# Kernel optimization log

Hardware: AMD Instinct MI355X
Metric: run time of the kernel (lower is better)

Reference implementation:

```python
import jax, jax.numpy as jnp
import numpy as np

# Model constants (from init_kwargs)
N_ATOMS = 30000
N_PAIRS = 300000
NF_IN = 64
NF_OUT = 64
N_DIST = 20
MIND_SOFT = 0.85
MAXD_SOFT = 5.0
HARD_CUTOFF = 6.5


def setup_inputs() -> dict:
    key = jax.random.key(0)
    k = jax.random.split(key, 8)
    in_features = jax.random.normal(k[0], (N_ATOMS, NF_IN), dtype=jnp.float32)
    pair_first = jax.random.randint(k[1], (N_PAIRS,), 0, N_ATOMS)
    pair_second = jax.random.randint(k[2], (N_PAIRS,), 0, N_ATOMS)
    dist_pairs = jax.random.uniform(k[3], (N_PAIRS,), dtype=jnp.float32,
                                    minval=MIND_SOFT, maxval=HARD_CUTOFF)
    # InverseSensitivityModule init: mu uniformly spaced in inverse-distance space
    mu = jnp.linspace(1.0 / MAXD_SOFT, 1.0 / MIND_SOFT, N_DIST, dtype=jnp.float32)
    sigma = jnp.full((N_DIST,), (1.0 / MIND_SOFT - 1.0 / MAXD_SOFT) / N_DIST,
                     dtype=jnp.float32)
    # xavier-normal-ish init scales
    int_weights = jax.random.normal(k[4], (N_DIST, NF_OUT, NF_IN), dtype=jnp.float32) \
        * np.sqrt(2.0 / (NF_IN + NF_OUT)).astype(np.float32)
    w_self = jax.random.normal(k[5], (NF_OUT, NF_IN), dtype=jnp.float32) \
        * np.sqrt(2.0 / (NF_IN + NF_OUT)).astype(np.float32)
    b_self = jax.random.normal(k[6], (NF_OUT,), dtype=jnp.float32) * 0.01
    return {"in_features": in_features, "pair_first": pair_first,
            "pair_second": pair_second, "dist_pairs": dist_pairs,
            "mu": mu, "sigma": sigma, "int_weights": int_weights,
            "w_self": w_self, "b_self": b_self}


def _sensitivity(dist, mu, sigma):
    # Inverse-distance Gaussian sensitivities with smooth cosine hard cutoff.
    inv_d = 1.0 / dist  # [P]
    gauss = jnp.exp(-0.5 * ((inv_d[:, None] - mu[None, :]) / sigma[None, :]) ** 2)  # [P, n_dist]
    cut = jnp.cos(0.5 * jnp.pi * dist / HARD_CUTOFF) ** 2
    cut = jnp.where(dist < HARD_CUTOFF, cut, 0.0)
    return gauss * cut[:, None]


def reference(in_features, pair_first, pair_second, dist_pairs,
              mu, sigma, int_weights, w_self, b_self):
    n_atoms = in_features.shape[0]
    sense = _sensitivity(dist_pairs, mu, sigma)              # [P, n_dist]
    # envsum: env[a, nu, f] = sum_{p: pair_first[p]==a} sense[p, nu] * in_features[pair_second[p], f]
    neigh = in_features[pair_second]                          # [P, nf_in] gather
    contrib = sense[:, :, None] * neigh[:, None, :]           # [P, n_dist, nf_in]
    env = jax.ops.segment_sum(
        contrib.reshape(contrib.shape[0], N_DIST * NF_IN),
        pair_first, num_segments=n_atoms)                     # [A, n_dist*nf_in]
    # interaction matmul: weights permuted (n_dist, nf_in, nf_out) then flattened
    weights_rs = jnp.transpose(int_weights, (0, 2, 1)).reshape(N_DIST * NF_IN, NF_OUT)
    features_out = env @ weights_rs                           # [A, nf_out]
    features_out += in_features @ w_self.T + b_self           # self interaction
    return features_out
```

## Files before the change

### kernel.cpp

```cpp
#include <hip/hip_runtime.h>
#include <math.h>

#define N_ATOMS    30000
#define N_PAIRS    300000
#define CAP        48
#define NF         64
#define ND         20
#define K_ENV      1280
#define K_TOT      1344
#define NKSTEP     42
#define BA         8
#define ESTRIDE    1352
#define D_LO       0.85f
#define D_SCALE    (5.65f / 65535.0f)
#define D_SCALE_I  (65535.0f / 5.65f)
#define NM1        ((unsigned)(N_ATOMS - 1))
#define PAD_WORD   0x0000FFFFu
#define GCONST     0.8493218f

typedef short    s16x8  __attribute__((ext_vector_type(8)));
typedef __bf16   bf16x8 __attribute__((ext_vector_type(8)));
typedef unsigned u32x4  __attribute__((ext_vector_type(4)));
typedef float    f32x4  __attribute__((ext_vector_type(4)));
typedef float    f32x16 __attribute__((ext_vector_type(16)));

__device__ __forceinline__ unsigned short f2bf(float x) {
    union { float f; unsigned u; } v; v.f = x;
    unsigned r = v.u + 0x7fffu + ((v.u >> 16) & 1u);
    return (unsigned short)(r >> 16);
}
__device__ __forceinline__ unsigned pkbf(float a, float b) {
    return (unsigned)f2bf(a) | ((unsigned)f2bf(b) << 16);
}
__device__ __forceinline__ unsigned pkrh(float a, float b) {
    unsigned ua = __builtin_bit_cast(unsigned, a) + 0x8000u;
    unsigned ub = __builtin_bit_cast(unsigned, b) + 0x8000u;
    return __builtin_amdgcn_perm(ub, ua, 0x07060302u);
}
__device__ __forceinline__ float senseq(unsigned pu, float slog, float nms) {
    float uf  = (float)(pu & 0xffffu);
    float d   = __builtin_fmaf(uf, D_SCALE, D_LO);
    float inv = __builtin_amdgcn_rcpf(d);
    float rev = __builtin_fmaf(uf, (float)(D_SCALE / 13.0f), D_LO / 13.0f);
    float cut = __builtin_fmaf(__builtin_amdgcn_cosf(rev), 0.5f, 0.5f);
    float zs  = __builtin_fmaf(inv, slog, nms);
    return __builtin_amdgcn_exp2f(-(zs * zs)) * cut;
}

__global__ void k_prep(const float* __restrict__ iw, const float* __restrict__ wself,
                       const float* __restrict__ mu, const float* __restrict__ sigma,
                       const float* __restrict__ x,
                       unsigned short* __restrict__ WtB, int* __restrict__ cnts,
                       float2* __restrict__ msr, unsigned* __restrict__ xb16,
                       unsigned* __restrict__ pk) {
    if (blockIdx.x < 42) {
        int idx = blockIdx.x * 256 + threadIdx.x;
        if (idx >= NKSTEP * 4 * 64) return;
        int l  = idx & 63;
        int q  = (idx >> 6) & 3;
        int ks = idx >> 8;
        int n  = q * 16 + (l & 15);
        int kb = ks * 32 + (l >> 4) * 8;
        u32x4 u;
        #pragma unroll
        for (int jj = 0; jj < 4; jj++) {
            unsigned short lo, hi;
            #pragma unroll
            for (int e = 0; e < 2; e++) {
                int k = kb + 2 * jj + e;
                float val;
                if (k < K_ENV) {
                    int t  = k / 640;
                    int rm = k - t * 640;
                    int g  = rm >> 7;
                    int c  = (rm & 127) >> 2;
                    int r  = k & 3;
                    int nu = 4 * g + r;
                    int f  = 2 * c + t;
                    val = iw[(nu * NF + n) * NF + f];
                } else {
                    val = wself[n * NF + (k - K_ENV)];
                }
                if (e == 0) lo = f2bf(val); else hi = f2bf(val);
            }
            u[jj] = (unsigned)lo | ((unsigned)hi << 16);
        }
        *(u32x4*)&WtB[idx * 8] = u;
    } else if (blockIdx.x < 160) {
        int i = (blockIdx.x - 42) * 256 + threadIdx.x;
        if (i < N_ATOMS) cnts[i] = 0;
    } else if (blockIdx.x == 160) {
        int i = threadIdx.x;
        if (i < ND) {
            float isg = 1.0f / sigma[i];
            float2 m;
            m.y = isg * GCONST;
            m.x = -mu[i] * isg * GCONST;
            msr[i] = m;
        }
    } else if (blockIdx.x < 1099) {
        int o = (blockIdx.x - 161) * 256 + threadIdx.x;
        if (o < N_ATOMS * 32 / 4) {
            int wbase = o * 4;
            const float* src = &x[(size_t)wbase * 2];
            float2 f0 = *(const float2*)(src);
            float2 f1 = *(const float2*)(src + 2);
            float2 f2 = *(const float2*)(src + 4);
            float2 f3 = *(const float2*)(src + 6);
            u32x4 u;
            u[0] = pkbf(f0.x, f0.y);
            u[1] = pkbf(f1.x, f1.y);
            u[2] = pkbf(f2.x, f2.y);
            u[3] = pkbf(f3.x, f3.y);
            *(u32x4*)&xb16[wbase] = u;
        }
    } else {
        int o = (blockIdx.x - 1099) * 256 + threadIdx.x;
        if (o < N_ATOMS * CAP / 4) {
            u32x4 u = {PAD_WORD, PAD_WORD, PAD_WORD, PAD_WORD};
            *(u32x4*)&pk[(size_t)o * 4] = u;
        }
    }
}

__global__ void k_scatter(const int* __restrict__ first, const int* __restrict__ second,
                          const float* __restrict__ dist, int* __restrict__ cnts,
                          unsigned* __restrict__ pk) {
    int p = (blockIdx.x * 256 + threadIdx.x) * 2;
    if (p >= N_PAIRS) return;
    int2   f2 = *(const int2*)&first[p];
    int2   s2 = *(const int2*)&second[p];
    float2 d2 = *(const float2*)&dist[p];
    {
        int pos = atomicAdd(&cnts[f2.x], 1);
        if (pos < CAP) {
            unsigned du = min((unsigned)((d2.x - D_LO) * D_SCALE_I + 0.5f), 65535u);
            pk[(size_t)f2.x * CAP + pos] = ((unsigned)s2.x << 16) | du;
        }
    }
    {
        int pos = atomicAdd(&cnts[f2.y], 1);
        if (pos < CAP) {
            unsigned du = min((unsigned)((d2.y - D_LO) * D_SCALE_I + 0.5f), 65535u);
            pk[(size_t)f2.y * CAP + pos] = ((unsigned)s2.y << 16) | du;
        }
    }
}

__global__ void __launch_bounds__(512, 6)
k_main(const unsigned* __restrict__ xb16, const int* __restrict__ cnts,
       const unsigned* __restrict__ pk, const float2* __restrict__ msr,
       const unsigned short* __restrict__ WtB, const float* __restrict__ bself,
       float* __restrict__ out) {
    __shared__ unsigned short env[BA * ESTRIDE];
    const int t  = threadIdx.x;
    const int w  = t >> 6;
    const int l  = t & 63;
    const int h  = l >> 5;
    const int cl = l & 31;
    const int a  = blockIdx.x * BA + w;

    float2 ms = msr[min(cl, ND - 1)];
    const float slog = ms.y;
    const float nms  = ms.x;
    const unsigned* xw = xb16 + cl;

    const int cnt = min(cnts[a], CAP);
    const int nst = (cnt + 15) >> 4;
    const unsigned* gb = &pk[(size_t)a * CAP];
    f32x16 acc0 = {0.f}, acc1 = {0.f};
    #pragma unroll 1
    for (int ks = 0; ks < nst; ks++) {
        const int k0 = ks * 16 + h * 8;
        uint4 p0 = *(const uint4*)(gb + k0);
        uint4 p1 = *(const uint4*)(gb + k0 + 4);
        unsigned g0 = xw[min(p0.x >> 16, NM1) * 32];
        unsigned g1 = xw[min(p0.y >> 16, NM1) * 32];
        unsigned g2 = xw[min(p0.z >> 16, NM1) * 32];
        unsigned g3 = xw[min(p0.w >> 16, NM1) * 32];
        unsigned g4 = xw[min(p1.x >> 16, NM1) * 32];
        unsigned g5 = xw[min(p1.y >> 16, NM1) * 32];
        unsigned g6 = xw[min(p1.z >> 16, NM1) * 32];
        unsigned g7 = xw[min(p1.w >> 16, NM1) * 32];
        u32x4 A, B0, B1;
        A[0] = pkrh(senseq(p0.x, slog, nms), senseq(p0.y, slog, nms));
        A[1] = pkrh(senseq(p0.z, slog, nms), senseq(p0.w, slog, nms));
        A[2] = pkrh(senseq(p1.x, slog, nms), senseq(p1.y, slog, nms));
        A[3] = pkrh(senseq(p1.z, slog, nms), senseq(p1.w, slog, nms));
        B0[0] = __builtin_amdgcn_perm(g1, g0, 0x05040100u);
        B0[1] = __builtin_amdgcn_perm(g3, g2, 0x05040100u);
        B0[2] = __builtin_amdgcn_perm(g5, g4, 0x05040100u);
        B0[3] = __builtin_amdgcn_perm(g7, g6, 0x05040100u);
        B1[0] = __builtin_amdgcn_perm(g1, g0, 0x07060302u);
        B1[1] = __builtin_amdgcn_perm(g3, g2, 0x07060302u);
        B1[2] = __builtin_amdgcn_perm(g5, g4, 0x07060302u);
        B1[3] = __builtin_amdgcn_perm(g7, g6, 0x07060302u);
        acc0 = __builtin_amdgcn_mfma_f32_32x32x16_bf16(
                   __builtin_bit_cast(bf16x8, A),
                   __builtin_bit_cast(bf16x8, B0), acc0, 0, 0, 0);
        acc1 = __builtin_amdgcn_mfma_f32_32x32x16_bf16(
                   __builtin_bit_cast(bf16x8, A),
                   __builtin_bit_cast(bf16x8, B1), acc1, 0, 0, 0);
    }
    unsigned short* er = &env[w * ESTRIDE];
    #pragma unroll
    for (int q = 0; q < 3; q++) {
        int g = 2 * q + h;
        if (g < 5) {
            uint2 v0, v1;
            v0.x = pkrh(acc0[4 * q + 0], acc0[4 * q + 1]);
            v0.y = pkrh(acc0[4 * q + 2], acc0[4 * q + 3]);
            v1.x = pkrh(acc1[4 * q + 0], acc1[4 * q + 1]);
            v1.y = pkrh(acc1[4 * q + 2], acc1[4 * q + 3]);
            *(uint2*)&er[g * 128 + cl * 4]       = v0;
            *(uint2*)&er[640 + g * 128 + cl * 4] = v1;
        }
    }
    unsigned sw = xb16[(size_t)a * 32 + (l >> 1)];
    er[K_ENV + l] = (unsigned short)(sw >> ((l & 1) * 16));
    __syncthreads();

    if (w < 4) {
        const int m16  = l & 15;
        const int quad = l >> 4;
        f32x4 acc = {0.f, 0.f, 0.f, 0.f};
        for (int ks = 0; ks < NKSTEP; ks++) {
            s16x8 afrag = *(const s16x8*)&env[(m16 & 7) * ESTRIDE + ks * 32 + quad * 8];
            s16x8 bfrag = *(const s16x8*)&WtB[((ks * 4 + w) * 64 + l) * 8];
            acc = __builtin_amdgcn_mfma_f32_16x16x32_bf16(
                      __builtin_bit_cast(bf16x8, afrag),
                      __builtin_bit_cast(bf16x8, bfrag), acc, 0, 0, 0);
        }
        const float bs = bself[w * 16 + m16];
        const int a0 = blockIdx.x * BA;
        #pragma unroll
        for (int r = 0; r < 4; r++) {
            int row = quad * 4 + r;
            if (row < BA)
                out[(size_t)(a0 + row) * NF + w * 16 + m16] = acc[r] + bs;
        }
    }
}

extern "C" void kernel_launch(void* const* d_in, const int* in_sizes, int n_in,
                              void* d_out, int out_size, void* d_ws, size_t ws_size,
                              hipStream_t stream) {
    const float* x      = (const float*)d_in[0];
    const int*   first  = (const int*)d_in[1];
    const int*   second = (const int*)d_in[2];
    const float* dist   = (const float*)d_in[3];
    const float* mu     = (const float*)d_in[4];
    const float* sigma  = (const float*)d_in[5];
    const float* iw     = (const float*)d_in[6];
    const float* wself  = (const float*)d_in[7];
    const float* bself  = (const float*)d_in[8];
    float* out = (float*)d_out;

    char* ws = (char*)d_ws;
    unsigned short* WtB  = (unsigned short*)(ws);
    int*            cnts = (int*)(ws + 172032);
    float2*         msr  = (float2*)(ws + 292032);
    unsigned*       pk   = (unsigned*)(ws + 292192);
    unsigned*       xb16 = (unsigned*)(ws + 6052192);

    k_prep<<<dim3(1099 + (N_ATOMS * CAP / 4 + 255) / 256), dim3(256), 0, stream>>>(
        iw, wself, mu, sigma, x, WtB, cnts, msr, xb16, pk);
    k_scatter<<<dim3((N_PAIRS / 2 + 255) / 256), dim3(256), 0, stream>>>(
        first, second, dist, cnts, pk);
    k_main<<<dim3(N_ATOMS / BA), dim3(512), 0, stream>>>(
        xb16, cnts, pk, msr, WtB, bself, out);
}
```

Before: 130.9 us.

## Use persistent blocks with atomic tile queue, 16-atom tiles, and masked padding

The main kernel now runs a fixed grid of persistent blocks that pull 16-atom tiles from an atomic counter. Each wave builds environments for two atoms, so the second-stage 16x16 MFMA uses all 16 rows instead of 8. The per-call pass that wrote 0xFFFF padding words into the neighbour list is removed; sensitivities for slots past each atom's count are zeroed in registers instead. This saves a large memset and wasted MFMA rows, at the cost of an extra atomic and barrier per tile and larger shared memory per block.

Result: slower. 190.7 us (+45.7%).

```diff
diff --git a/kernel.cpp b/kernel.cpp
--- a/kernel.cpp
+++ b/kernel.cpp
@@ -9,13 +9,14 @@
 #define K_ENV      1280
 #define K_TOT      1344
 #define NKSTEP     42
-#define BA         8
+#define BA         16
+#define NTILE      1875
+#define NBLK       768
 #define ESTRIDE    1352
 #define D_LO       0.85f
 #define D_SCALE    (5.65f / 65535.0f)
 #define D_SCALE_I  (65535.0f / 5.65f)
 #define NM1        ((unsigned)(N_ATOMS - 1))
-#define PAD_WORD   0x0000FFFFu
 #define GCONST     0.8493218f
 
 typedef short    s16x8  __attribute__((ext_vector_type(8)));
@@ -37,14 +38,16 @@
     unsigned ub = __builtin_bit_cast(unsigned, b) + 0x8000u;
     return __builtin_amdgcn_perm(ub, ua, 0x07060302u);
 }
-__device__ __forceinline__ float senseq(unsigned pu, float slog, float nms) {
+__device__ __forceinline__ float senseq(unsigned pu, int kidx, int cnt,
+                                        float slog, float nms) {
     float uf  = (float)(pu & 0xffffu);
     float d   = __builtin_fmaf(uf, D_SCALE, D_LO);
     float inv = __builtin_amdgcn_rcpf(d);
     float rev = __builtin_fmaf(uf, (float)(D_SCALE / 13.0f), D_LO / 13.0f);
     float cut = __builtin_fmaf(__builtin_amdgcn_cosf(rev), 0.5f, 0.5f);
     float zs  = __builtin_fmaf(inv, slog, nms);
-    return __builtin_amdgcn_exp2f(-(zs * zs)) * cut;
+    float e   = __builtin_amdgcn_exp2f(-(zs * zs)) * cut;
+    return (kidx < cnt) ? e : 0.0f;
 }
 
 __global__ void k_prep(const float* __restrict__ iw, const float* __restrict__ wself,
@@ -52,7 +55,7 @@
                        const float* __restrict__ x,
                        unsigned short* __restrict__ WtB, int* __restrict__ cnts,
                        float2* __restrict__ msr, unsigned* __restrict__ xb16,
-                       unsigned* __restrict__ pk) {
+                       int* __restrict__ ctr) {
     if (blockIdx.x < 42) {
         int idx = blockIdx.x * 256 + threadIdx.x;
         if (idx >= NKSTEP * 4 * 64) return;
@@ -98,7 +101,8 @@
             m.x = -mu[i] * isg * GCONST;
             msr[i] = m;
         }
-    } else if (blockIdx.x < 1099) {
+        if (i == 0) *ctr = NBLK;
+    } else {
         int o = (blockIdx.x - 161) * 256 + threadIdx.x;
         if (o < N_ATOMS * 32 / 4) {
             int wbase = o * 4;
@@ -114,12 +118,6 @@
             u[3] = pkbf(f3.x, f3.y);
             *(u32x4*)&xb16[wbase] = u;
         }
-    } else {
-        int o = (blockIdx.x - 1099) * 256 + threadIdx.x;
-        if (o < N_ATOMS * CAP / 4) {
-            u32x4 u = {PAD_WORD, PAD_WORD, PAD_WORD, PAD_WORD};
-            *(u32x4*)&pk[(size_t)o * 4] = u;
-        }
     }
 }
 
@@ -151,94 +149,110 @@
 k_main(const unsigned* __restrict__ xb16, const int* __restrict__ cnts,
        const unsigned* __restrict__ pk, const float2* __restrict__ msr,
        const unsigned short* __restrict__ WtB, const float* __restrict__ bself,
-       float* __restrict__ out) {
+       float* __restrict__ out, int* __restrict__ ctr) {
     __shared__ unsigned short env[BA * ESTRIDE];
+    __shared__ int tile_s;
     const int t  = threadIdx.x;
     const int w  = t >> 6;
     const int l  = t & 63;
     const int h  = l >> 5;
     const int cl = l & 31;
-    const int a  = blockIdx.x * BA + w;
+    const int m16  = l & 15;
+    const int quad = l >> 4;
 
     float2 ms = msr[min(cl, ND - 1)];
     const float slog = ms.y;
     const float nms  = ms.x;
     const unsigned* xw = xb16 + cl;
-
-    const int cnt = min(cnts[a], CAP);
-    const int nst = (cnt + 15) >> 4;
-    const unsigned* gb = &pk[(size_t)a * CAP];
-    f32x16 acc0 = {0.f}, acc1 = {0.f};
-    #pragma unroll 1
-    for (int ks = 0; ks < nst; ks++) {
-        const int k0 = ks * 16 + h * 8;
-        uint4 p0 = *(const uint4*)(gb + k0);
-        uint4 p1 = *(const uint4*)(gb + k0 + 4);
-        unsigned g0 = xw[min(p0.x >> 16, NM1) * 32];
-        unsigned g1 = xw[min(p0.y >> 16, NM1) * 32];
-        unsigned g2 = xw[min(p0.z >> 16, NM1) * 32];
-        unsigned g3 = xw[min(p0.w >> 16, NM1) * 32];
-        unsigned g4 = xw[min(p1.x >> 16, NM1) * 32];
-        unsigned g5 = xw[min(p1.y >> 16, NM1) * 32];
-        unsigned g6 = xw[min(p1.z >> 16, NM1) * 32];
-        unsigned g7 = xw[min(p1.w >> 16, NM1) * 32];
-        u32x4 A, B0, B1;
-        A[0] = pkrh(senseq(p0.x, slog, nms), senseq(p0.y, slog, nms));
-        A[1] = pkrh(senseq(p0.z, slog, nms), senseq(p0.w, slog, nms));
-        A[2] = pkrh(senseq(p1.x, slog, nms), senseq(p1.y, slog, nms));
-        A[3] = pkrh(senseq(p1.z, slog, nms), senseq(p1.w, slog, nms));
-        B0[0] = __builtin_amdgcn_perm(g1, g0, 0x05040100u);
-        B0[1] = __builtin_amdgcn_perm(g3, g2, 0x05040100u);
-        B0[2] = __builtin_amdgcn_perm(g5, g4, 0x05040100u);
-        B0[3] = __builtin_amdgcn_perm(g7, g6, 0x05040100u);
-        B1[0] = __builtin_amdgcn_perm(g1, g0, 0x07060302u);
-        B1[1] = __builtin_amdgcn_perm(g3, g2, 0x07060302u);
-        B1[2] = __builtin_amdgcn_perm(g5, g4, 0x07060302u);
-        B1[3] = __builtin_amdgcn_perm(g7, g6, 0x07060302u);
-        acc0 = __builtin_amdgcn_mfma_f32_32x32x16_bf16(
-                   __builtin_bit_cast(bf16x8, A),
-                   __builtin_bit_cast(bf16x8, B0), acc0, 0, 0, 0);
-        acc1 = __builtin_amdgcn_mfma_f32_32x32x16_bf16(
-                   __builtin_bit_cast(bf16x8, A),
-                   __builtin_bit_cast(bf16x8, B1), acc1, 0, 0, 0);
-    }
-    unsigned short* er = &env[w * ESTRIDE];
-    #pragma unroll
-    for (int q = 0; q < 3; q++) {
-        int g = 2 * q + h;
-        if (g < 5) {
-            uint2 v0, v1;
-            v0.x = pkrh(acc0[4 * q + 0], acc0[4 * q + 1]);
-            v0.y = pkrh(acc0[4 * q + 2], acc0[4 * q + 3]);
-            v1.x = pkrh(acc1[4 * q + 0], acc1[4 * q + 1]);
-            v1.y = pkrh(acc1[4 * q + 2], acc1[4 * q + 3]);
-            *(uint2*)&er[g * 128 + cl * 4]       = v0;
-            *(uint2*)&er[640 + g * 128 + cl * 4] = v1;
-        }
-    }
-    unsigned sw = xb16[(size_t)a * 32 + (l >> 1)];
-    er[K_ENV + l] = (unsigned short)(sw >> ((l & 1) * 16));
-    __syncthreads();
-
-    if (w < 4) {
-        const int m16  = l & 15;
-        const int quad = l >> 4;
-        f32x4 acc = {0.f, 0.f, 0.f, 0.f};
-        for (int ks = 0; ks < NKSTEP; ks++) {
-            s16x8 afrag = *(const s16x8*)&env[(m16 & 7) * ESTRIDE + ks * 32 + quad * 8];
-            s16x8 bfrag = *(const s16x8*)&WtB[((ks * 4 + w) * 64 + l) * 8];
-            acc = __builtin_amdgcn_mfma_f32_16x16x32_bf16(
-                      __builtin_bit_cast(bf16x8, afrag),
-                      __builtin_bit_cast(bf16x8, bfrag), acc, 0, 0, 0);
-        }
-        const float bs = bself[w * 16 + m16];
-        const int a0 = blockIdx.x * BA;
-        #pragma unroll
-        for (int r = 0; r < 4; r++) {
-            int row = quad * 4 + r;
-            if (row < BA)
+    const float bs = bself[(w & 3) * 16 + m16];
+
+    int tile = blockIdx.x;
+    while (tile < NTILE) {
+        const int a0 = tile * BA;
+
+        #pragma unroll 1
+        for (int ci = 0; ci < 2; ci++) {
+            const int i = 2 * w + ci;
+            const int a = a0 + i;
+            const int cnt = min(cnts[a], CAP);
+            const int nst = (cnt + 15) >> 4;
+            const unsigned* gb = &pk[(size_t)a * CAP];
+            f32x16 acc0 = {0.f}, acc1 = {0.f};
+            #pragma unroll 1
+            for (int ks = 0; ks < nst; ks++) {
+                const int k0 = ks * 16 + h * 8;
+                uint4 p0 = *(const uint4*)(gb + k0);
+                uint4 p1 = *(const uint4*)(gb + k0 + 4);
+                unsigned g0 = xw[min(p0.x >> 16, NM1) * 32];
+                unsigned g1 = xw[min(p0.y >> 16, NM1) * 32];
+                unsigned g2 = xw[min(p0.z >> 16, NM1) * 32];
+                unsigned g3 = xw[min(p0.w >> 16, NM1) * 32];
+                unsigned g4 = xw[min(p1.x >> 16, NM1) * 32];
+                unsigned g5 = xw[min(p1.y >> 16, NM1) * 32];
+                unsigned g6 = xw[min(p1.z >> 16, NM1) * 32];
+                unsigned g7 = xw[min(p1.w >> 16, NM1) * 32];
+                u32x4 A, B0, B1;
+                A[0] = pkrh(senseq(p0.x, k0 + 0, cnt, slog, nms),
+                            senseq(p0.y, k0 + 1, cnt, slog, nms));
+                A[1] = pkrh(senseq(p0.z, k0 + 2, cnt, slog, nms),
+                            senseq(p0.w, k0 + 3, cnt, slog, nms));
+                A[2] = pkrh(senseq(p1.x, k0 + 4, cnt, slog, nms),
+                            senseq(p1.y, k0 + 5, cnt, slog, nms));
+                A[3] = pkrh(senseq(p1.z, k0 + 6, cnt, slog, nms),
+                            senseq(p1.w, k0 + 7, cnt, slog, nms));
+                B0[0] = __builtin_amdgcn_perm(g1, g0, 0x05040100u);
+                B0[1] = __builtin_amdgcn_perm(g3, g2, 0x05040100u);
+                B0[2] = __builtin_amdgcn_perm(g5, g4, 0x05040100u);
+                B0[3] = __builtin_amdgcn_perm(g7, g6, 0x05040100u);
+                B1[0] = __builtin_amdgcn_perm(g1, g0, 0x07060302u);
+                B1[1] = __builtin_amdgcn_perm(g3, g2, 0x07060302u);
+                B1[2] = __builtin_amdgcn_perm(g5, g4, 0x07060302u);
+                B1[3] = __builtin_amdgcn_perm(g7, g6, 0x07060302u);
+                acc0 = __builtin_amdgcn_mfma_f32_32x32x16_bf16(
+                           __builtin_bit_cast(bf16x8, A),
+                           __builtin_bit_cast(bf16x8, B0), acc0, 0, 0, 0);
+                acc1 = __builtin_amdgcn_mfma_f32_32x32x16_bf16(
+                           __builtin_bit_cast(bf16x8, A),
+                           __builtin_bit_cast(bf16x8, B1), acc1, 0, 0, 0);
+            }
+            unsigned short* er = &env[i * ESTRIDE];
+            #pragma unroll
+            for (int q = 0; q < 3; q++) {
+                int g = 2 * q + h;
+                if (g < 5) {
+                    uint2 v0, v1;
+                    v0.x = pkrh(acc0[4 * q + 0], acc0[4 * q + 1]);
+                    v0.y = pkrh(acc0[4 * q + 2], acc0[4 * q + 3]);
+                    v1.x = pkrh(acc1[4 * q + 0], acc1[4 * q + 1]);
+                    v1.y = pkrh(acc1[4 * q + 2], acc1[4 * q + 3]);
+                    *(uint2*)&er[g * 128 + cl * 4]       = v0;
+                    *(uint2*)&er[640 + g * 128 + cl * 4] = v1;
+                }
+            }
+            unsigned sw = xb16[(size_t)a * 32 + (l >> 1)];
+            er[K_ENV + l] = (unsigned short)(sw >> ((l & 1) * 16));
+        }
+        __syncthreads();
+
+        if (w < 4) {
+            f32x4 acc = {0.f, 0.f, 0.f, 0.f};
+            for (int ks = 0; ks < NKSTEP; ks++) {
+                s16x8 afrag = *(const s16x8*)&env[m16 * ESTRIDE + ks * 32 + quad * 8];
+                s16x8 bfrag = *(const s16x8*)&WtB[((ks * 4 + w) * 64 + l) * 8];
+                acc = __builtin_amdgcn_mfma_f32_16x16x32_bf16(
+                          __builtin_bit_cast(bf16x8, afrag),
+                          __builtin_bit_cast(bf16x8, bfrag), acc, 0, 0, 0);
+            }
+            #pragma unroll
+            for (int r = 0; r < 4; r++) {
+                int row = quad * 4 + r;
                 out[(size_t)(a0 + row) * NF + w * 16 + m16] = acc[r] + bs;
-        }
+            }
+        }
+
+        if (t == 0) tile_s = atomicAdd(ctr, 1);
+        __syncthreads();
+        tile = tile_s;
     }
 }
 
@@ -260,13 +274,14 @@
     unsigned short* WtB  = (unsigned short*)(ws);
     int*            cnts = (int*)(ws + 172032);
     float2*         msr  = (float2*)(ws + 292032);
-    unsigned*       pk   = (unsigned*)(ws + 292192);
-    unsigned*       xb16 = (unsigned*)(ws + 6052192);
-
-    k_prep<<<dim3(1099 + (N_ATOMS * CAP / 4 + 255) / 256), dim3(256), 0, stream>>>(
-        iw, wself, mu, sigma, x, WtB, cnts, msr, xb16, pk);
+    int*            ctr  = (int*)(ws + 292192);
+    unsigned*       pk   = (unsigned*)(ws + 292256);
+    unsigned*       xb16 = (unsigned*)(ws + 6052256);
+
+    k_prep<<<dim3(161 + (N_ATOMS * 8 + 255) / 256), dim3(256), 0, stream>>>(
+        iw, wself, mu, sigma, x, WtB, cnts, msr, xb16, ctr);
     k_scatter<<<dim3((N_PAIRS / 2 + 255) / 256), dim3(256), 0, stream>>>(
         first, second, dist, cnts, pk);
-    k_main<<<dim3(N_ATOMS / BA), dim3(512), 0, stream>>>(
-        xb16, cnts, pk, msr, WtB, bself, out);
-}
+    k_main<<<dim3(NBLK), dim3(512), 0, stream>>>(
+        xb16, cnts, pk, msr, WtB, bself, out, ctr);
+}
```
